# Optimization experiments

Measured on AMD Instinct MI355X. Metric: run time of the kernel, lower is better.

## Reference

```python
import jax, jax.numpy as jnp
import numpy as np

B, D, H, O, E = 4096, 1024, 4096, 1024, 8
TOP_K = 2


def setup_inputs() -> dict:
    key = jax.random.key(0)
    ks = jax.random.split(key, 7)
    s = 0.02
    return {
        "expert_input": jax.random.normal(ks[0], (B, D), dtype=jnp.float32),
        "Wg": jax.random.normal(ks[1], (D, E), dtype=jnp.float32) * s,
        "bg": jnp.zeros((E,), dtype=jnp.float32),
        "W1": jax.random.normal(ks[2], (E, D, H), dtype=jnp.float32) * s,
        "b1": jnp.zeros((E, H), dtype=jnp.float32),
        "W2": jax.random.normal(ks[3], (E, H, O), dtype=jnp.float32) * s,
        "b2": jnp.zeros((E, O), dtype=jnp.float32),
    }


def reference(expert_input, Wg, bg, W1, b1, W2, b2):
    x = expert_input                                  # [B, D]
    gate_logits = x @ Wg + bg                         # [B, E]
    topk_logits, topk_idx = jax.lax.top_k(gate_logits, TOP_K)
    topk_w = jax.nn.softmax(topk_logits, axis=1)      # softmax over the k selected logits
    rows = jnp.arange(x.shape[0])[:, None]
    dense_w = jnp.zeros_like(gate_logits).at[rows, topk_idx].set(topk_w)  # [B, E]
    # Dense (all-experts) evaluation; zero gate weight == unrouted, so math
    # matches the masked per-expert loop in the torch module exactly.
    h = jax.nn.relu(jnp.einsum('bd,edh->ebh', x, W1) + b1[:, None, :])    # [E, B, H]
    expert_out = jnp.einsum('ebh,eho->ebo', h, W2) + b2[:, None, :]       # [E, B, O]
    routed = jnp.einsum('be,ebo->bo', dense_w, expert_out)                # [B, O]
    return routed
```

## Files before the change

kernel.cpp:

```cpp
#include <hip/hip_runtime.h>
#include <cstdint>

#define DEVI __device__ __forceinline__

typedef __bf16 bf16x8_t __attribute__((ext_vector_type(8)));
typedef float f32x4_t __attribute__((ext_vector_type(4)));

typedef const __attribute__((address_space(1))) unsigned int* gas_t;
typedef __attribute__((address_space(3))) unsigned int* las_t;

DEVI void glds16(const void* g, void* l) {
  __builtin_amdgcn_global_load_lds((gas_t)g, (las_t)l, 16, 0, 0);
}

DEVI uint16_t f2b(float f) {
  uint32_t u = __builtin_bit_cast(uint32_t, f);
  u += 0x7fffu + ((u >> 16) & 1u);
  return (uint16_t)(u >> 16);
}

static constexpr int MAXT = 72;

__global__ __launch_bounds__(256) void moe_gate(const float* __restrict__ x,
    const float* __restrict__ Wg, const float* __restrict__ bg,
    int* __restrict__ gidx, float* __restrict__ gw) {
  const int lane = threadIdx.x & 63;
  const int b = blockIdx.x * 4 + (threadIdx.x >> 6);
  float acc[8];
#pragma unroll
  for (int e = 0; e < 8; ++e) acc[e] = 0.f;
  const float* xr = x + (size_t)b * 1024;
#pragma unroll
  for (int it = 0; it < 4; ++it) {
    const int d0 = it * 256 + lane * 4;
    float4 xv = *(const float4*)(xr + d0);
    float xs[4] = {xv.x, xv.y, xv.z, xv.w};
#pragma unroll
    for (int q = 0; q < 4; ++q) {
      const float4* wrow = (const float4*)(Wg + (size_t)(d0 + q) * 8);
      float4 wa = wrow[0], wb = wrow[1];
      acc[0] += xs[q] * wa.x; acc[1] += xs[q] * wa.y;
      acc[2] += xs[q] * wa.z; acc[3] += xs[q] * wa.w;
      acc[4] += xs[q] * wb.x; acc[5] += xs[q] * wb.y;
      acc[6] += xs[q] * wb.z; acc[7] += xs[q] * wb.w;
    }
  }
#pragma unroll
  for (int off = 32; off; off >>= 1)
#pragma unroll
    for (int e = 0; e < 8; ++e) acc[e] += __shfl_xor(acc[e], off, 64);
  if (lane == 0) {
    float l[8];
#pragma unroll
    for (int e = 0; e < 8; ++e) l[e] = acc[e] + bg[e];
    int i0 = 0;
#pragma unroll
    for (int e = 1; e < 8; ++e) if (l[e] > l[i0]) i0 = e;
    int i1 = (i0 == 0) ? 1 : 0;
#pragma unroll
    for (int e = 0; e < 8; ++e) if (e != i0 && l[e] > l[i1]) i1 = e;
    float ex = expf(l[i1] - l[i0]);
    float s = 1.f + ex;
    gidx[2 * b] = i0; gidx[2 * b + 1] = i1;
    gw[2 * b] = 1.f / s; gw[2 * b + 1] = ex / s;
  }
}

__global__ __launch_bounds__(256) void moe_scan(const int* __restrict__ gidx,
                                                int* __restrict__ meta) {
  __shared__ int cnt[8];
  if (threadIdx.x < 8) cnt[threadIdx.x] = 0;
  __syncthreads();
  int loc[8] = {0, 0, 0, 0, 0, 0, 0, 0};
  for (int i = threadIdx.x; i < 8192; i += 256) {
    int e = gidx[i];
#pragma unroll
    for (int q = 0; q < 8; ++q) loc[q] += (e == q) ? 1 : 0;
  }
#pragma unroll
  for (int q = 0; q < 8; ++q) atomicAdd(&cnt[q], loc[q]);
  __syncthreads();
  if (threadIdx.x == 0) {
    int off = 0, t = 0;
    for (int e = 0; e < 8; ++e) {
      int c = cnt[e];
      meta[e] = c;
      meta[8 + e] = off;
      meta[17 + e] = 0;
      int nt = (c + 127) >> 7;
      for (int mt = 0; mt < nt; ++mt) {
        meta[32 + t] = e;
        meta[104 + t] = off + mt * 128;
        meta[176 + t] = off + c;
        ++t;
      }
      off += c;
    }
    meta[16] = off;
    meta[25] = t;
  }
}

__global__ __launch_bounds__(256) void moe_scatter(const int* __restrict__ gidx,
    const float* __restrict__ gw, int* __restrict__ meta,
    int* __restrict__ row_index, float* __restrict__ row_w) {
  int i = blockIdx.x * 256 + threadIdx.x;
  int e = gidx[i];
  int pos = meta[8 + e] + atomicAdd(&meta[17 + e], 1);
  row_index[pos] = i >> 1;
  row_w[pos] = gw[i];
}

__global__ __launch_bounds__(256) void moe_cvtx(const float* __restrict__ x,
                                                uint16_t* __restrict__ xb) {
  size_t i = ((size_t)blockIdx.x * 256 + threadIdx.x) * 4;
  float4 v = *(const float4*)(x + i);
  uint64_t pk = (uint64_t)f2b(v.x) | ((uint64_t)f2b(v.y) << 16) |
                ((uint64_t)f2b(v.z) << 32) | ((uint64_t)f2b(v.w) << 48);
  *(uint64_t*)(xb + i) = pk;
}

__global__ __launch_bounds__(256) void moe_transpose(const float* __restrict__ in,
                                                     uint16_t* __restrict__ outp,
                                                     int K, int N) {
  __shared__ uint16_t t[64][72];
  const int e = blockIdx.z;
  const int k0 = blockIdx.y * 64, n0 = blockIdx.x * 64;
  const int r = threadIdx.x >> 2;
  const int c0 = (threadIdx.x & 3) * 16;
  const float* src = in + ((size_t)e * K + k0 + r) * N + n0 + c0;
#pragma unroll
  for (int q = 0; q < 4; ++q) {
    float4 v = *(const float4*)(src + q * 4);
    uint64_t pk = (uint64_t)f2b(v.x) | ((uint64_t)f2b(v.y) << 16) |
                  ((uint64_t)f2b(v.z) << 32) | ((uint64_t)f2b(v.w) << 48);
    *(uint64_t*)&t[r][c0 + q * 4] = pk;
  }
  __syncthreads();
  alignas(16) uint16_t buf[16];
#pragma unroll
  for (int j = 0; j < 16; ++j) buf[j] = t[c0 + j][r];
  uint16_t* dst = outp + ((size_t)e * N + n0 + r) * K + k0 + c0;
  *(uint4*)dst = *(const uint4*)&buf[0];
  *(uint4*)(dst + 8) = *(const uint4*)&buf[8];
}

template <int KD, int ND, int MODE>
__global__ __launch_bounds__(256, 4) void moe_gemm(
    const uint16_t* __restrict__ Am, const uint16_t* __restrict__ Bt,
    const float* __restrict__ bias, const int* __restrict__ meta,
    const int* __restrict__ row_index, const float* __restrict__ row_w,
    uint16_t* __restrict__ hout, float* __restrict__ out) {
  constexpr int NB = ND / 128;
  const int nwg = gridDim.x;
  const int orig = blockIdx.x;
  const int q8 = nwg >> 3, r8 = nwg & 7, xcd = orig & 7, loc = orig >> 3;
  int wg = (xcd < r8 ? xcd * (q8 + 1) : r8 * (q8 + 1) + (xcd - r8) * q8) + loc;
  const int nb = wg % NB;
  const int ty = wg / NB;
  if (ty >= meta[25]) return;
  const int e = meta[32 + ty];
  const int pos0 = meta[104 + ty];
  const int vend = meta[176 + ty];

  __shared__ uint16_t As[2][128 * 32];
  __shared__ uint16_t Bs[2][128 * 32];

  const int tid = threadIdx.x;
  const int lane = tid & 63;
  const int w = tid >> 6;
  const int wr = w >> 1, wc = w & 1;

  size_t aoff[2], boff[2];
#pragma unroll
  for (int j = 0; j < 2; ++j) {
    int c = j * 256 + tid;
    int row = c >> 2;
    int skc = (c & 3) ^ ((row >> 1) & 3);
    int pos = pos0 + row;
    if (pos > 8191) pos = 8191;
    int ar = (MODE == 1) ? row_index[pos] : pos;
    aoff[j] = ((size_t)ar * KD + (size_t)skc * 8) * 2;
    boff[j] = (((size_t)e * ND + (size_t)nb * 128 + row) * KD + (size_t)skc * 8) * 2;
  }
  const char* Ag = (const char*)Am;
  const char* Bg = (const char*)Bt;

  f32x4_t acc[4][4];
  f32x4_t z;
  z[0] = 0.f; z[1] = 0.f; z[2] = 0.f; z[3] = 0.f;
#pragma unroll
  for (int m = 0; m < 4; ++m)
#pragma unroll
    for (int n = 0; n < 4; ++n) acc[m][n] = z;

  auto stage = [&](int buf, int t) {
#pragma unroll
    for (int j = 0; j < 2; ++j) {
      glds16(Ag + aoff[j] + (size_t)t * 64, &As[buf][(j * 256 + w * 64) * 8]);
      glds16(Bg + boff[j] + (size_t)t * 64, &Bs[buf][(j * 256 + w * 64) * 8]);
    }
  };

  stage(0, 0);
  __syncthreads();
  int cur = 0;
  const int NIT = KD / 32;
  for (int t = 0; t < NIT; ++t) {
    if (t + 1 < NIT) stage(cur ^ 1, t + 1);
    const uint16_t* Ap = As[cur];
    const uint16_t* Bp = Bs[cur];
    bf16x8_t af[4], bfr[4];
#pragma unroll
    for (int m = 0; m < 4; ++m) {
      int row = wr * 64 + m * 16 + (lane & 15);
      int skc = ((lane >> 4) ^ (row >> 1)) & 3;
      af[m] = *(const bf16x8_t*)(Ap + row * 32 + skc * 8);
    }
#pragma unroll
    for (int n = 0; n < 4; ++n) {
      int row = wc * 64 + n * 16 + (lane & 15);
      int skc = ((lane >> 4) ^ (row >> 1)) & 3;
      bfr[n] = *(const bf16x8_t*)(Bp + row * 32 + skc * 8);
    }
#pragma unroll
    for (int m = 0; m < 4; ++m)
#pragma unroll
      for (int n = 0; n < 4; ++n)
        acc[m][n] = __builtin_amdgcn_mfma_f32_16x16x32_bf16(af[m], bfr[n], acc[m][n], 0, 0, 0);
    __syncthreads();
    cur ^= 1;
  }

  const int cb = nb * 128 + wc * 64;
  if constexpr (MODE == 1) {
#pragma unroll
    for (int m = 0; m < 4; ++m) {
      int pr = pos0 + wr * 64 + m * 16 + ((lane >> 4) << 2);
#pragma unroll
      for (int i = 0; i < 4; ++i) {
        int pos = pr + i;
        if (pos < vend) {
#pragma unroll
          for (int n = 0; n < 4; ++n) {
            int col = cb + n * 16 + (lane & 15);
            float v = acc[m][n][i] + bias[e * ND + col];
            v = fmaxf(v, 0.f);
            hout[(size_t)pos * ND + col] = f2b(v);
          }
        }
      }
    }
  } else {
#pragma unroll
    for (int m = 0; m < 4; ++m) {
      int pr = pos0 + wr * 64 + m * 16 + ((lane >> 4) << 2);
#pragma unroll
      for (int i = 0; i < 4; ++i) {
        int pos = pr + i;
        if (pos < vend) {
          int bi = row_index[pos];
          float wgt = row_w[pos];
          float* orow = out + (size_t)bi * ND;
#pragma unroll
          for (int n = 0; n < 4; ++n) {
            int col = cb + n * 16 + (lane & 15);
            float v = (acc[m][n][i] + bias[e * ND + col]) * wgt;
            atomicAdd(orow + col, v);
          }
        }
      }
    }
  }
}

extern "C" void kernel_launch(void* const* d_in, const int* in_sizes, int n_in,
                              void* d_out, int out_size, void* d_ws, size_t ws_size,
                              hipStream_t stream) {
  const float* x  = (const float*)d_in[0];
  const float* Wg = (const float*)d_in[1];
  const float* bg = (const float*)d_in[2];
  const float* W1 = (const float*)d_in[3];
  const float* b1 = (const float*)d_in[4];
  const float* W2 = (const float*)d_in[5];
  const float* b2 = (const float*)d_in[6];
  float* out = (float*)d_out;

  char* ws = (char*)d_ws;
  uint16_t* w1t = (uint16_t*)ws; ws += (size_t)8 * 4096 * 1024 * 2;
  uint16_t* w2t = (uint16_t*)ws; ws += (size_t)8 * 1024 * 4096 * 2;
  uint16_t* xb  = (uint16_t*)ws; ws += (size_t)4096 * 1024 * 2;
  uint16_t* h   = (uint16_t*)ws; ws += (size_t)8192 * 4096 * 2;
  int*   gidx = (int*)ws;   ws += 8192 * 4;
  float* gw   = (float*)ws; ws += 8192 * 4;
  int*   rix  = (int*)ws;   ws += 8192 * 4;
  float* rw   = (float*)ws; ws += 8192 * 4;
  int*   meta = (int*)ws;   ws += 4096;

  hipMemsetAsync(d_out, 0, (size_t)4096 * 1024 * 4, stream);
  moe_cvtx<<<4096, 256, 0, stream>>>(x, xb);
  moe_transpose<<<dim3(4096 / 64, 1024 / 64, 8), 256, 0, stream>>>(W1, w1t, 1024, 4096);
  moe_transpose<<<dim3(1024 / 64, 4096 / 64, 8), 256, 0, stream>>>(W2, w2t, 4096, 1024);
  moe_gate<<<1024, 256, 0, stream>>>(x, Wg, bg, gidx, gw);
  moe_scan<<<1, 256, 0, stream>>>(gidx, meta);
  moe_scatter<<<32, 256, 0, stream>>>(gidx, gw, meta, rix, rw);
  moe_gemm<1024, 4096, 1><<<dim3(32 * MAXT), 256, 0, stream>>>(xb, w1t, b1, meta, rix, rw, h, nullptr);
  moe_gemm<4096, 1024, 2><<<dim3(8 * MAXT), 256, 0, stream>>>(h, w2t, b2, meta, rix, rw, nullptr, out);
}
```

Before: 431.7 us.

## Deepen MoE GEMM LDS pipeline to four stages with inline-asm fragment loads

Result: slower. 477.5 us (+10.6%).

```diff
diff --git a/kernel.cpp b/kernel.cpp
--- a/kernel.cpp
+++ b/kernel.cpp
@@ -17,6 +17,21 @@
   uint32_t u = __builtin_bit_cast(uint32_t, f);
   u += 0x7fffu + ((u >> 16) & 1u);
   return (uint16_t)(u >> 16);
+}
+
+DEVI f32x4_t ldsr(uint32_t addr) {
+  f32x4_t r;
+  asm volatile("ds_read_b128 %0, %1" : "=v"(r) : "v"(addr));
+  return r;
+}
+DEVI f32x4_t ldsr_o(uint32_t addr, int imm) {
+  f32x4_t r;
+  switch (imm) {
+    case 1024: asm volatile("ds_read_b128 %0, %1 offset:1024" : "=v"(r) : "v"(addr)); break;
+    case 2048: asm volatile("ds_read_b128 %0, %1 offset:2048" : "=v"(r) : "v"(addr)); break;
+    default:   asm volatile("ds_read_b128 %0, %1 offset:3072" : "=v"(r) : "v"(addr)); break;
+  }
+  return r;
 }
 
 static constexpr int MAXT = 72;
@@ -152,6 +167,7 @@
     const int* __restrict__ row_index, const float* __restrict__ row_w,
     uint16_t* __restrict__ hout, float* __restrict__ out) {
   constexpr int NB = ND / 128;
+  extern __shared__ uint16_t lds[];
   const int nwg = gridDim.x;
   const int orig = blockIdx.x;
   const int q8 = nwg >> 3, r8 = nwg & 7, xcd = orig & 7, loc = orig >> 3;
@@ -163,9 +179,6 @@
   const int pos0 = meta[104 + ty];
   const int vend = meta[176 + ty];
 
-  __shared__ uint16_t As[2][128 * 32];
-  __shared__ uint16_t Bs[2][128 * 32];
-
   const int tid = threadIdx.x;
   const int lane = tid & 63;
   const int w = tid >> 6;
@@ -186,6 +199,16 @@
   const char* Ag = (const char*)Am;
   const char* Bg = (const char*)Bt;
 
+  auto stage = [&](int s, int kt) {
+    uint16_t* Adst = lds + s * 4096;
+    uint16_t* Bdst = lds + 16384 + s * 4096;
+#pragma unroll
+    for (int j = 0; j < 2; ++j) {
+      glds16(Ag + aoff[j] + (size_t)kt * 64, Adst + (j * 256 + w * 64) * 8);
+      glds16(Bg + boff[j] + (size_t)kt * 64, Bdst + (j * 256 + w * 64) * 8);
+    }
+  };
+
   f32x4_t acc[4][4];
   f32x4_t z;
   z[0] = 0.f; z[1] = 0.f; z[2] = 0.f; z[3] = 0.f;
@@ -194,43 +217,41 @@
 #pragma unroll
     for (int n = 0; n < 4; ++n) acc[m][n] = z;
 
-  auto stage = [&](int buf, int t) {
-#pragma unroll
-    for (int j = 0; j < 2; ++j) {
-      glds16(Ag + aoff[j] + (size_t)t * 64, &As[buf][(j * 256 + w * 64) * 8]);
-      glds16(Bg + boff[j] + (size_t)t * 64, &Bs[buf][(j * 256 + w * 64) * 8]);
-    }
-  };
-
-  stage(0, 0);
-  __syncthreads();
-  int cur = 0;
+  const int skcf = ((lane >> 4) ^ ((lane & 15) >> 1)) & 3;
+  const uint32_t lbase = (uint32_t)(size_t)&lds[0];
+  const uint32_t aFrag = lbase + (uint32_t)(wr * 64 * 32 + (lane & 15) * 32 + skcf * 8) * 2;
+  const uint32_t bFrag = lbase + 32768 + (uint32_t)(wc * 64 * 32 + (lane & 15) * 32 + skcf * 8) * 2;
+
+  stage(0, 0); stage(1, 1); stage(2, 2);
+  asm volatile("s_waitcnt vmcnt(8)" ::: "memory");
+  __builtin_amdgcn_s_barrier();
+
   const int NIT = KD / 32;
   for (int t = 0; t < NIT; ++t) {
-    if (t + 1 < NIT) stage(cur ^ 1, t + 1);
-    const uint16_t* Ap = As[cur];
-    const uint16_t* Bp = Bs[cur];
-    bf16x8_t af[4], bfr[4];
-#pragma unroll
-    for (int m = 0; m < 4; ++m) {
-      int row = wr * 64 + m * 16 + (lane & 15);
-      int skc = ((lane >> 4) ^ (row >> 1)) & 3;
-      af[m] = *(const bf16x8_t*)(Ap + row * 32 + skc * 8);
-    }
-#pragma unroll
-    for (int n = 0; n < 4; ++n) {
-      int row = wc * 64 + n * 16 + (lane & 15);
-      int skc = ((lane >> 4) ^ (row >> 1)) & 3;
-      bfr[n] = *(const bf16x8_t*)(Bp + row * 32 + skc * 8);
-    }
+    int tc = t + 3; if (tc > NIT - 1) tc = NIT - 1;
+    stage((t + 3) & 3, tc);
+
+    const uint32_t sA = aFrag + (uint32_t)((t & 3) * 8192);
+    const uint32_t sB = bFrag + (uint32_t)((t & 3) * 8192);
+    f32x4_t a0 = ldsr(sA), a1 = ldsr_o(sA, 1024), a2 = ldsr_o(sA, 2048), a3 = ldsr_o(sA, 3072);
+    f32x4_t b0 = ldsr(sB), b1 = ldsr_o(sB, 1024), b2 = ldsr_o(sB, 2048), b3 = ldsr_o(sB, 3072);
+    asm volatile("s_waitcnt lgkmcnt(0)" ::: "memory");
+    __builtin_amdgcn_sched_barrier(0);
+
+    bf16x8_t af[4] = {__builtin_bit_cast(bf16x8_t, a0), __builtin_bit_cast(bf16x8_t, a1),
+                      __builtin_bit_cast(bf16x8_t, a2), __builtin_bit_cast(bf16x8_t, a3)};
+    bf16x8_t bfr[4] = {__builtin_bit_cast(bf16x8_t, b0), __builtin_bit_cast(bf16x8_t, b1),
+                       __builtin_bit_cast(bf16x8_t, b2), __builtin_bit_cast(bf16x8_t, b3)};
 #pragma unroll
     for (int m = 0; m < 4; ++m)
 #pragma unroll
       for (int n = 0; n < 4; ++n)
         acc[m][n] = __builtin_amdgcn_mfma_f32_16x16x32_bf16(af[m], bfr[n], acc[m][n], 0, 0, 0);
-    __syncthreads();
-    cur ^= 1;
-  }
+
+    asm volatile("s_waitcnt vmcnt(8)" ::: "memory");
+    __builtin_amdgcn_s_barrier();
+  }
+  asm volatile("s_waitcnt vmcnt(0)" ::: "memory");
 
   const int cb = nb * 128 + wc * 64;
   if constexpr (MODE == 1) {
@@ -297,6 +318,11 @@
   float* rw   = (float*)ws; ws += 8192 * 4;
   int*   meta = (int*)ws;   ws += 4096;
 
+  hipFuncSetAttribute((const void*)moe_gemm<1024, 4096, 1>,
+                      hipFuncAttributeMaxDynamicSharedMemorySize, 65536);
+  hipFuncSetAttribute((const void*)moe_gemm<4096, 1024, 2>,
+                      hipFuncAttributeMaxDynamicSharedMemorySize, 65536);
+
   hipMemsetAsync(d_out, 0, (size_t)4096 * 1024 * 4, stream);
   moe_cvtx<<<4096, 256, 0, stream>>>(x, xb);
   moe_transpose<<<dim3(4096 / 64, 1024 / 64, 8), 256, 0, stream>>>(W1, w1t, 1024, 4096);
@@ -304,6 +330,6 @@
   moe_gate<<<1024, 256, 0, stream>>>(x, Wg, bg, gidx, gw);
   moe_scan<<<1, 256, 0, stream>>>(gidx, meta);
   moe_scatter<<<32, 256, 0, stream>>>(gidx, gw, meta, rix, rw);
-  moe_gemm<1024, 4096, 1><<<dim3(32 * MAXT), 256, 0, stream>>>(xb, w1t, b1, meta, rix, rw, h, nullptr);
-  moe_gemm<4096, 1024, 2><<<dim3(8 * MAXT), 256, 0, stream>>>(h, w2t, b2, meta, rix, rw, nullptr, out);
-}
+  moe_gemm<1024, 4096, 1><<<dim3(32 * MAXT), 256, 65536, stream>>>(xb, w1t, b1, meta, rix, rw, h, nullptr);
+  moe_gemm<4096, 1024, 2><<<dim3(8 * MAXT), 256, 65536, stream>>>(h, w2t, b2, meta, rix, rw, nullptr, out);
+}
```

## Retile MoE GEMMs to 128x256 tiles with K64 steps and split-K for down-projection

Applied to the files above, without the earlier changes.

New measurement: 534.3 us. 1.24x slower.

```diff
diff --git a/kernel.cpp b/kernel.cpp
--- a/kernel.cpp
+++ b/kernel.cpp
@@ -17,6 +17,20 @@
   uint32_t u = __builtin_bit_cast(uint32_t, f);
   u += 0x7fffu + ((u >> 16) & 1u);
   return (uint16_t)(u >> 16);
+}
+
+template <int IMM>
+DEVI f32x4_t ldsr(uint32_t addr) {
+  f32x4_t r;
+  if constexpr (IMM == 0)
+    asm volatile("ds_read_b128 %0, %1" : "=v"(r) : "v"(addr));
+  else if constexpr (IMM == 2048)
+    asm volatile("ds_read_b128 %0, %1 offset:2048" : "=v"(r) : "v"(addr));
+  else if constexpr (IMM == 4096)
+    asm volatile("ds_read_b128 %0, %1 offset:4096" : "=v"(r) : "v"(addr));
+  else
+    asm volatile("ds_read_b128 %0, %1 offset:6144" : "=v"(r) : "v"(addr));
+  return r;
 }
 
 static constexpr int MAXT = 72;
@@ -145,94 +159,125 @@
   *(uint4*)(dst + 8) = *(const uint4*)&buf[8];
 }
 
-template <int KD, int ND, int MODE>
-__global__ __launch_bounds__(256, 4) void moe_gemm(
+template <int KD, int ND, int MODE, int KSL, int NBQ>
+__global__ __launch_bounds__(512, 2) void moe_gemm(
     const uint16_t* __restrict__ Am, const uint16_t* __restrict__ Bt,
     const float* __restrict__ bias, const int* __restrict__ meta,
     const int* __restrict__ row_index, const float* __restrict__ row_w,
     uint16_t* __restrict__ hout, float* __restrict__ out) {
-  constexpr int NB = ND / 128;
+  constexpr int KSLEN = KD / KSL;
+  constexpr int NIT = KSLEN / 64;
+  extern __shared__ uint16_t lds[];
+
   const int nwg = gridDim.x;
   const int orig = blockIdx.x;
   const int q8 = nwg >> 3, r8 = nwg & 7, xcd = orig & 7, loc = orig >> 3;
   int wg = (xcd < r8 ? xcd * (q8 + 1) : r8 * (q8 + 1) + (xcd - r8) * q8) + loc;
-  const int nb = wg % NB;
-  const int ty = wg / NB;
+  const int nb_lo = wg & 3; wg >>= 2;
+  const int ty = wg % MAXT; wg /= MAXT;
+  const int sgrp = wg % NBQ;
+  const int ks = wg / NBQ;
+  const int nb = sgrp * 4 + nb_lo;
   if (ty >= meta[25]) return;
   const int e = meta[32 + ty];
   const int pos0 = meta[104 + ty];
   const int vend = meta[176 + ty];
-
-  __shared__ uint16_t As[2][128 * 32];
-  __shared__ uint16_t Bs[2][128 * 32];
+  const int k0 = ks * KSLEN;
 
   const int tid = threadIdx.x;
   const int lane = tid & 63;
   const int w = tid >> 6;
-  const int wr = w >> 1, wc = w & 1;
-
-  size_t aoff[2], boff[2];
-#pragma unroll
-  for (int j = 0; j < 2; ++j) {
-    int c = j * 256 + tid;
-    int row = c >> 2;
-    int skc = (c & 3) ^ ((row >> 1) & 3);
-    int pos = pos0 + row;
-    if (pos > 8191) pos = 8191;
+  const int wr = w >> 2, wc = w & 3;
+
+  size_t aoff[2], boff[4];
+#pragma unroll
+  for (int i = 0; i < 2; ++i) {
+    int c = (w * 2 + i) * 64 + lane;
+    int row = c >> 3;
+    int gc = (c & 7) ^ (row & 7);
+    int pos = pos0 + row; if (pos > 8191) pos = 8191;
     int ar = (MODE == 1) ? row_index[pos] : pos;
-    aoff[j] = ((size_t)ar * KD + (size_t)skc * 8) * 2;
-    boff[j] = (((size_t)e * ND + (size_t)nb * 128 + row) * KD + (size_t)skc * 8) * 2;
+    aoff[i] = ((size_t)ar * KD + k0 + gc * 8) * 2;
+  }
+#pragma unroll
+  for (int i = 0; i < 4; ++i) {
+    int c = (w * 4 + i) * 64 + lane;
+    int row = c >> 3;
+    int gc = (c & 7) ^ (row & 7);
+    boff[i] = (((size_t)e * ND + (size_t)nb * 256 + row) * KD + k0 + gc * 8) * 2;
   }
   const char* Ag = (const char*)Am;
   const char* Bg = (const char*)Bt;
 
+  auto stage = [&](int kt, int buf) {
+    uint16_t* base = lds + buf * 32768;
+#pragma unroll
+    for (int i = 0; i < 2; ++i)
+      glds16(Ag + aoff[i] + (size_t)kt * 128, base + (w * 2 + i) * 512);
+#pragma unroll
+    for (int i = 0; i < 4; ++i)
+      glds16(Bg + boff[i] + (size_t)kt * 128, base + 8192 + (w * 4 + i) * 512);
+  };
+
   f32x4_t acc[4][4];
-  f32x4_t z;
-  z[0] = 0.f; z[1] = 0.f; z[2] = 0.f; z[3] = 0.f;
+  f32x4_t z; z[0] = 0.f; z[1] = 0.f; z[2] = 0.f; z[3] = 0.f;
 #pragma unroll
   for (int m = 0; m < 4; ++m)
 #pragma unroll
     for (int n = 0; n < 4; ++n) acc[m][n] = z;
 
-  auto stage = [&](int buf, int t) {
-#pragma unroll
-    for (int j = 0; j < 2; ++j) {
-      glds16(Ag + aoff[j] + (size_t)t * 64, &As[buf][(j * 256 + w * 64) * 8]);
-      glds16(Bg + boff[j] + (size_t)t * 64, &Bs[buf][(j * 256 + w * 64) * 8]);
-    }
-  };
+  const uint32_t lbase = (uint32_t)(size_t)&lds[0];
+  const uint32_t slot0 = (uint32_t)(((lane >> 4) ^ (lane & 7)) & 7);
+  const uint32_t aRd = lbase + (uint32_t)((wr * 64 + (lane & 15)) * 128) + slot0 * 16;
+  const uint32_t bRd = lbase + 16384 + (uint32_t)((wc * 64 + (lane & 15)) * 128) + slot0 * 16;
 
   stage(0, 0);
-  __syncthreads();
-  int cur = 0;
-  const int NIT = KD / 32;
+  asm volatile("s_waitcnt vmcnt(0)" ::: "memory");
+  __builtin_amdgcn_s_barrier();
+
   for (int t = 0; t < NIT; ++t) {
-    if (t + 1 < NIT) stage(cur ^ 1, t + 1);
-    const uint16_t* Ap = As[cur];
-    const uint16_t* Bp = Bs[cur];
-    bf16x8_t af[4], bfr[4];
-#pragma unroll
-    for (int m = 0; m < 4; ++m) {
-      int row = wr * 64 + m * 16 + (lane & 15);
-      int skc = ((lane >> 4) ^ (row >> 1)) & 3;
-      af[m] = *(const bf16x8_t*)(Ap + row * 32 + skc * 8);
-    }
-#pragma unroll
-    for (int n = 0; n < 4; ++n) {
-      int row = wc * 64 + n * 16 + (lane & 15);
-      int skc = ((lane >> 4) ^ (row >> 1)) & 3;
-      bfr[n] = *(const bf16x8_t*)(Bp + row * 32 + skc * 8);
-    }
+    int tc = t + 1; if (tc > NIT - 1) tc = NIT - 1;
+    stage(tc, (t + 1) & 1);
+
+    const uint32_t bo = (t & 1) ? 65536u : 0u;
+    const uint32_t aA = aRd + bo, bA = bRd + bo;
+    const uint32_t aB = aA ^ 64u, bB = bA ^ 64u;
+
+    f32x4_t xa0[4], yb0[4], xa1[4], yb1[4];
+    xa0[0] = ldsr<0>(aA); xa0[1] = ldsr<2048>(aA); xa0[2] = ldsr<4096>(aA); xa0[3] = ldsr<6144>(aA);
+    yb0[0] = ldsr<0>(bA); yb0[1] = ldsr<2048>(bA); yb0[2] = ldsr<4096>(bA); yb0[3] = ldsr<6144>(bA);
+    xa1[0] = ldsr<0>(aB); xa1[1] = ldsr<2048>(aB); xa1[2] = ldsr<4096>(aB); xa1[3] = ldsr<6144>(aB);
+    yb1[0] = ldsr<0>(bB); yb1[1] = ldsr<2048>(bB); yb1[2] = ldsr<4096>(bB); yb1[3] = ldsr<6144>(bB);
+
+    asm volatile("s_waitcnt lgkmcnt(8)" ::: "memory");
+    __builtin_amdgcn_sched_barrier(0);
+    __builtin_amdgcn_s_setprio(1);
 #pragma unroll
     for (int m = 0; m < 4; ++m)
 #pragma unroll
       for (int n = 0; n < 4; ++n)
-        acc[m][n] = __builtin_amdgcn_mfma_f32_16x16x32_bf16(af[m], bfr[n], acc[m][n], 0, 0, 0);
-    __syncthreads();
-    cur ^= 1;
-  }
-
-  const int cb = nb * 128 + wc * 64;
+        acc[m][n] = __builtin_amdgcn_mfma_f32_16x16x32_bf16(
+            __builtin_bit_cast(bf16x8_t, xa0[m]), __builtin_bit_cast(bf16x8_t, yb0[n]),
+            acc[m][n], 0, 0, 0);
+    __builtin_amdgcn_s_setprio(0);
+
+    asm volatile("s_waitcnt lgkmcnt(0)" ::: "memory");
+    __builtin_amdgcn_sched_barrier(0);
+    __builtin_amdgcn_s_setprio(1);
+#pragma unroll
+    for (int m = 0; m < 4; ++m)
+#pragma unroll
+      for (int n = 0; n < 4; ++n)
+        acc[m][n] = __builtin_amdgcn_mfma_f32_16x16x32_bf16(
+            __builtin_bit_cast(bf16x8_t, xa1[m]), __builtin_bit_cast(bf16x8_t, yb1[n]),
+            acc[m][n], 0, 0, 0);
+    __builtin_amdgcn_s_setprio(0);
+
+    asm volatile("s_waitcnt vmcnt(0)" ::: "memory");
+    __builtin_amdgcn_s_barrier();
+  }
+
+  const int cb = nb * 256 + wc * 64;
   if constexpr (MODE == 1) {
 #pragma unroll
     for (int m = 0; m < 4; ++m) {
@@ -265,8 +310,8 @@
 #pragma unroll
           for (int n = 0; n < 4; ++n) {
             int col = cb + n * 16 + (lane & 15);
-            float v = (acc[m][n][i] + bias[e * ND + col]) * wgt;
-            atomicAdd(orow + col, v);
+            float bterm = (ks == 0) ? bias[e * ND + col] : 0.f;
+            atomicAdd(orow + col, (acc[m][n][i] + bterm) * wgt);
           }
         }
       }
@@ -297,6 +342,11 @@
   float* rw   = (float*)ws; ws += 8192 * 4;
   int*   meta = (int*)ws;   ws += 4096;
 
+  hipFuncSetAttribute((const void*)moe_gemm<1024, 4096, 1, 1, 4>,
+                      hipFuncAttributeMaxDynamicSharedMemorySize, 131072);
+  hipFuncSetAttribute((const void*)moe_gemm<4096, 1024, 2, 4, 1>,
+                      hipFuncAttributeMaxDynamicSharedMemorySize, 131072);
+
   hipMemsetAsync(d_out, 0, (size_t)4096 * 1024 * 4, stream);
   moe_cvtx<<<4096, 256, 0, stream>>>(x, xb);
   moe_transpose<<<dim3(4096 / 64, 1024 / 64, 8), 256, 0, stream>>>(W1, w1t, 1024, 4096);
@@ -304,6 +354,8 @@
   moe_gate<<<1024, 256, 0, stream>>>(x, Wg, bg, gidx, gw);
   moe_scan<<<1, 256, 0, stream>>>(gidx, meta);
   moe_scatter<<<32, 256, 0, stream>>>(gidx, gw, meta, rix, rw);
-  moe_gemm<1024, 4096, 1><<<dim3(32 * MAXT), 256, 0, stream>>>(xb, w1t, b1, meta, rix, rw, h, nullptr);
-  moe_gemm<4096, 1024, 2><<<dim3(8 * MAXT), 256, 0, stream>>>(h, w2t, b2, meta, rix, rw, nullptr, out);
-}
+  moe_gemm<1024, 4096, 1, 1, 4><<<dim3(1152), 512, 131072, stream>>>(
+      xb, w1t, b1, meta, rix, rw, h, nullptr);
+  moe_gemm<4096, 1024, 2, 4, 1><<<dim3(1152), 512, 131072, stream>>>(
+      h, w2t, b2, meta, rix, rw, nullptr, out);
+}
```

## Split-K the second expert GEMM and fuse x bf16 conversion into gate

Applied to the files above, without the earlier changes.

Result: slower. 477.8 us (+10.7%).

```diff
diff --git a/kernel.cpp b/kernel.cpp
--- a/kernel.cpp
+++ b/kernel.cpp
@@ -23,17 +23,21 @@
 
 __global__ __launch_bounds__(256) void moe_gate(const float* __restrict__ x,
     const float* __restrict__ Wg, const float* __restrict__ bg,
-    int* __restrict__ gidx, float* __restrict__ gw) {
+    int* __restrict__ gidx, float* __restrict__ gw, uint16_t* __restrict__ xb) {
   const int lane = threadIdx.x & 63;
   const int b = blockIdx.x * 4 + (threadIdx.x >> 6);
   float acc[8];
 #pragma unroll
   for (int e = 0; e < 8; ++e) acc[e] = 0.f;
   const float* xr = x + (size_t)b * 1024;
+  uint16_t* xbr = xb + (size_t)b * 1024;
 #pragma unroll
   for (int it = 0; it < 4; ++it) {
     const int d0 = it * 256 + lane * 4;
     float4 xv = *(const float4*)(xr + d0);
+    uint64_t pk = (uint64_t)f2b(xv.x) | ((uint64_t)f2b(xv.y) << 16) |
+                  ((uint64_t)f2b(xv.z) << 32) | ((uint64_t)f2b(xv.w) << 48);
+    *(uint64_t*)(xbr + d0) = pk;
     float xs[4] = {xv.x, xv.y, xv.z, xv.w};
 #pragma unroll
     for (int q = 0; q < 4; ++q) {
@@ -111,15 +115,6 @@
   row_w[pos] = gw[i];
 }
 
-__global__ __launch_bounds__(256) void moe_cvtx(const float* __restrict__ x,
-                                                uint16_t* __restrict__ xb) {
-  size_t i = ((size_t)blockIdx.x * 256 + threadIdx.x) * 4;
-  float4 v = *(const float4*)(x + i);
-  uint64_t pk = (uint64_t)f2b(v.x) | ((uint64_t)f2b(v.y) << 16) |
-                ((uint64_t)f2b(v.z) << 32) | ((uint64_t)f2b(v.w) << 48);
-  *(uint64_t*)(xb + i) = pk;
-}
-
 __global__ __launch_bounds__(256) void moe_transpose(const float* __restrict__ in,
                                                      uint16_t* __restrict__ outp,
                                                      int K, int N) {
@@ -145,23 +140,27 @@
   *(uint4*)(dst + 8) = *(const uint4*)&buf[8];
 }
 
-template <int KD, int ND, int MODE>
+template <int KD, int ND, int MODE, int KSL>
 __global__ __launch_bounds__(256, 4) void moe_gemm(
     const uint16_t* __restrict__ Am, const uint16_t* __restrict__ Bt,
     const float* __restrict__ bias, const int* __restrict__ meta,
     const int* __restrict__ row_index, const float* __restrict__ row_w,
     uint16_t* __restrict__ hout, float* __restrict__ out) {
   constexpr int NB = ND / 128;
+  constexpr int KSLEN = KD / KSL;
+  constexpr int NIT = KSLEN / 32;
   const int nwg = gridDim.x;
   const int orig = blockIdx.x;
   const int q8 = nwg >> 3, r8 = nwg & 7, xcd = orig & 7, loc = orig >> 3;
   int wg = (xcd < r8 ? xcd * (q8 + 1) : r8 * (q8 + 1) + (xcd - r8) * q8) + loc;
-  const int nb = wg % NB;
-  const int ty = wg / NB;
+  const int nb = wg % NB; wg /= NB;
+  const int ks = wg % KSL; wg /= KSL;
+  const int ty = wg;
   if (ty >= meta[25]) return;
   const int e = meta[32 + ty];
   const int pos0 = meta[104 + ty];
   const int vend = meta[176 + ty];
+  const int k0 = ks * KSLEN;
 
   __shared__ uint16_t As[2][128 * 32];
   __shared__ uint16_t Bs[2][128 * 32];
@@ -180,8 +179,8 @@
     int pos = pos0 + row;
     if (pos > 8191) pos = 8191;
     int ar = (MODE == 1) ? row_index[pos] : pos;
-    aoff[j] = ((size_t)ar * KD + (size_t)skc * 8) * 2;
-    boff[j] = (((size_t)e * ND + (size_t)nb * 128 + row) * KD + (size_t)skc * 8) * 2;
+    aoff[j] = ((size_t)ar * KD + (size_t)k0 + (size_t)skc * 8) * 2;
+    boff[j] = (((size_t)e * ND + (size_t)nb * 128 + row) * KD + (size_t)k0 + (size_t)skc * 8) * 2;
   }
   const char* Ag = (const char*)Am;
   const char* Bg = (const char*)Bt;
@@ -205,7 +204,6 @@
   stage(0, 0);
   __syncthreads();
   int cur = 0;
-  const int NIT = KD / 32;
   for (int t = 0; t < NIT; ++t) {
     if (t + 1 < NIT) stage(cur ^ 1, t + 1);
     const uint16_t* Ap = As[cur];
@@ -265,8 +263,8 @@
 #pragma unroll
           for (int n = 0; n < 4; ++n) {
             int col = cb + n * 16 + (lane & 15);
-            float v = (acc[m][n][i] + bias[e * ND + col]) * wgt;
-            atomicAdd(orow + col, v);
+            float bterm = (ks == 0) ? bias[e * ND + col] : 0.f;
+            atomicAdd(orow + col, (acc[m][n][i] + bterm) * wgt);
           }
         }
       }
@@ -298,12 +296,13 @@
   int*   meta = (int*)ws;   ws += 4096;
 
   hipMemsetAsync(d_out, 0, (size_t)4096 * 1024 * 4, stream);
-  moe_cvtx<<<4096, 256, 0, stream>>>(x, xb);
+  moe_gate<<<1024, 256, 0, stream>>>(x, Wg, bg, gidx, gw, xb);
   moe_transpose<<<dim3(4096 / 64, 1024 / 64, 8), 256, 0, stream>>>(W1, w1t, 1024, 4096);
   moe_transpose<<<dim3(1024 / 64, 4096 / 64, 8), 256, 0, stream>>>(W2, w2t, 4096, 1024);
-  moe_gate<<<1024, 256, 0, stream>>>(x, Wg, bg, gidx, gw);
   moe_scan<<<1, 256, 0, stream>>>(gidx, meta);
   moe_scatter<<<32, 256, 0, stream>>>(gidx, gw, meta, rix, rw);
-  moe_gemm<1024, 4096, 1><<<dim3(32 * MAXT), 256, 0, stream>>>(xb, w1t, b1, meta, rix, rw, h, nullptr);
-  moe_gemm<4096, 1024, 2><<<dim3(8 * MAXT), 256, 0, stream>>>(h, w2t, b2, meta, rix, rw, nullptr, out);
-}
+  moe_gemm<1024, 4096, 1, 1><<<dim3(32 * MAXT), 256, 0, stream>>>(
+      xb, w1t, b1, meta, rix, rw, h, nullptr);
+  moe_gemm<4096, 1024, 2, 2><<<dim3(8 * 2 * MAXT), 256, 0, stream>>>(
+      h, w2t, b2, meta, rix, rw, nullptr, out);
+}
```
